# Optimization experiments

Measured on AMD Instinct MI355X. Metric: run time of the kernel, lower is better.

## Reference

```python
import jax, jax.numpy as jnp
import numpy as np

N_NODES = 50000
N_EDGES = 800000
D = 64  # in_dim = hidden = out_dim
LEAKY_SLOPE = 0.01  # F.leaky_relu default


def gat_layer(h, src, dst, W, b, aW, ab):
    # fc: z = h @ W.T + b            [N, D_out]
    z = h @ W.T + b
    zs = z[src]                       # gather src feats  [E, D_out]
    zd = z[dst]                       # gather dst feats  [E, D_out]
    # attn_fc(concat(z_src, z_dst)) -> scalar per edge, then leaky_relu
    e = jnp.concatenate([zs, zd], axis=-1) @ aW.T + ab   # [E, 1]
    e = jax.nn.leaky_relu(e, LEAKY_SLOPE)[:, 0]          # [E]
    # softmax over incoming edges per destination node (mailbox softmax)
    m = jax.ops.segment_max(e, dst, num_segments=N_NODES)    # [N]
    ex = jnp.exp(e - m[dst])
    den = jax.ops.segment_sum(ex, dst, num_segments=N_NODES)  # [N]
    alpha = ex / den[dst]                                      # [E]
    # scatter-sum aggregate of alpha * z_src
    return jax.ops.segment_sum(alpha[:, None] * zs, dst, num_segments=N_NODES)


def setup_inputs() -> dict:
    key = jax.random.key(0)
    ks = jax.random.split(key, 16)
    x = jax.random.normal(ks[0], (N_NODES, D), dtype=jnp.float32)
    src = jax.random.randint(ks[1], (N_EDGES,), 0, N_NODES)
    dst = jax.random.randint(ks[2], (N_EDGES,), 0, N_NODES)
    # xavier_normal with relu gain, per reset_parameters
    gain = float(np.sqrt(2.0))
    params = {}
    for i in range(3):
        std_fc = gain * np.sqrt(2.0 / (D + D))
        std_at = gain * np.sqrt(2.0 / (2 * D + 1))
        params[f"W{i}"] = jax.random.normal(ks[3 + 4 * i], (D, D), dtype=jnp.float32) * std_fc
        params[f"b{i}"] = jnp.zeros((D,), dtype=jnp.float32)
        params[f"a{i}"] = jax.random.normal(ks[4 + 4 * i], (1, 2 * D), dtype=jnp.float32) * std_at
        params[f"ab{i}"] = jnp.zeros((1,), dtype=jnp.float32)
    return {"x": x, "src": src, "dst": dst, **params}


def reference(x, src, dst, W0, b0, a0, ab0, W1, b1, a1, ab1, W2, b2, a2, ab2):
    h = gat_layer(x, src, dst, W0, b0, a0, ab0)
    h = jax.nn.relu(h)
    h = gat_layer(h, src, dst, W1, b1, a1, ab1)
    h = jax.nn.relu(h)
    h = gat_layer(h, src, dst, W2, b2, a2, ab2)
    return h
```

## Files before the change

kernel.cpp:

```cpp
#include <hip/hip_runtime.h>
#include <math.h>

#define N_NODES 50000
#define N_EDGES 800000
#define D 64

#define NB 256
#define NBLK 256
#define BUCKET_NODES 196
#define TILE 3125

template<int N>
__global__ void scan_partial_g(const int* __restrict__ in, int* __restrict__ partials) {
    const int base = blockIdx.x * 1024 + threadIdx.x * 4;
    int4 c = make_int4(0, 0, 0, 0);
    if (base + 3 < N) c = *(const int4*)&in[base];
    else { int* cp = (int*)&c; for (int j = 0; j < 4; ++j) if (base + j < N) cp[j] = in[base + j]; }
    int s = c.x + c.y + c.z + c.w;
    #pragma unroll
    for (int off = 32; off >= 1; off >>= 1) s += __shfl_xor(s, off, 64);
    __shared__ int red[4];
    if ((threadIdx.x & 63) == 0) red[threadIdx.x >> 6] = s;
    __syncthreads();
    if (threadIdx.x == 0) partials[blockIdx.x] = red[0] + red[1] + red[2] + red[3];
}

__global__ void scan_offsets_g(int* __restrict__ partials, int nt, int* __restrict__ total_out) {
    const int lane = threadIdx.x;
    const int v = (lane < nt) ? partials[lane] : 0;
    int inc = v;
    #pragma unroll
    for (int off = 1; off < 64; off <<= 1) {
        const int w = __shfl_up(inc, off, 64);
        if (lane >= off) inc += w;
    }
    if (lane < nt) partials[lane] = inc - v;
    if (total_out != nullptr && lane == 63) *total_out = inc;
}

template<int N>
__global__ void scan_write_g(const int* __restrict__ in, const int* __restrict__ partials,
                             int* __restrict__ out) {
    const int tid  = threadIdx.x;
    const int base = blockIdx.x * 1024 + tid * 4;
    int4 c = make_int4(0, 0, 0, 0);
    if (base + 3 < N) c = *(const int4*)&in[base];
    else { int* cp = (int*)&c; for (int j = 0; j < 4; ++j) if (base + j < N) cp[j] = in[base + j]; }
    const int s = c.x + c.y + c.z + c.w;
    __shared__ int sh[256];
    sh[tid] = s;
    __syncthreads();
    for (int off = 1; off < 256; off <<= 1) {
        const int w = (tid >= off) ? sh[tid - off] : 0;
        __syncthreads();
        sh[tid] += w;
        __syncthreads();
    }
    int run = partials[blockIdx.x] + sh[tid] - s;
    const int* cp = (const int*)&c;
    int rp[4];
    #pragma unroll
    for (int j = 0; j < 4; ++j) { rp[j] = run; run += cp[j]; }
    if (base + 3 < N) *(int4*)&out[base] = make_int4(rp[0], rp[1], rp[2], rp[3]);
    else for (int j = 0; j < 4; ++j) if (base + j < N) out[base + j] = rp[j];
}

__global__ __launch_bounds__(256) void bucket_hist(const int* __restrict__ dst,
                                                   int* __restrict__ Acnt) {
    __shared__ int hist[NB];
    for (int i = threadIdx.x; i < NB; i += 256) hist[i] = 0;
    __syncthreads();
    const int base = blockIdx.x * TILE;
    for (int i = threadIdx.x; i < TILE; i += 256)
        atomicAdd(&hist[dst[base + i] / BUCKET_NODES], 1);
    __syncthreads();
    for (int bk = threadIdx.x; bk < NB; bk += 256)
        Acnt[bk * NBLK + blockIdx.x] = hist[bk];
}

__global__ __launch_bounds__(256) void bucket_scatter(const int* __restrict__ src,
                                                      const int* __restrict__ dst,
                                                      const int* __restrict__ offs,
                                                      int2* __restrict__ staging) {
    __shared__ int cur[NB];
    for (int i = threadIdx.x; i < NB; i += 256) cur[i] = offs[i * NBLK + blockIdx.x];
    __syncthreads();
    const int base = blockIdx.x * TILE;
    for (int i = threadIdx.x; i < TILE; i += 256) {
        const int s = src[base + i], d = dst[base + i];
        const int pos = atomicAdd(&cur[d / BUCKET_NODES], 1);
        staging[pos] = make_int2(s, d);
    }
}

__global__ __launch_bounds__(256) void node_counts(const int2* __restrict__ staging,
                                                   const int* __restrict__ offs,
                                                   int* __restrict__ counts) {
    __shared__ int cnt[BUCKET_NODES];
    const int b = blockIdx.x;
    for (int i = threadIdx.x; i < BUCKET_NODES; i += 256) cnt[i] = 0;
    __syncthreads();
    const int s0 = offs[b * NBLK];
    const int s1 = (b == NB - 1) ? N_EDGES : offs[(b + 1) * NBLK];
    for (int i = s0 + threadIdx.x; i < s1; i += 256)
        atomicAdd(&cnt[staging[i].y - b * BUCKET_NODES], 1);
    __syncthreads();
    for (int i = threadIdx.x; i < BUCKET_NODES; i += 256) {
        const int node = b * BUCKET_NODES + i;
        if (node < N_NODES) counts[node] = cnt[i];
    }
}

__global__ __launch_bounds__(256) void bucket_to_csr(const int2* __restrict__ staging,
                                                     const int* __restrict__ offs,
                                                     const int* __restrict__ row_ptr,
                                                     int* __restrict__ csr_src) {
    __shared__ int cur[BUCKET_NODES];
    const int b = blockIdx.x;
    for (int i = threadIdx.x; i < BUCKET_NODES; i += 256) {
        const int node = b * BUCKET_NODES + i;
        cur[i] = (node < N_NODES) ? row_ptr[node] : 0;
    }
    __syncthreads();
    const int s0 = offs[b * NBLK];
    const int s1 = (b == NB - 1) ? N_EDGES : offs[(b + 1) * NBLK];
    for (int i = s0 + threadIdx.x; i < s1; i += 256) {
        const int2 e = staging[i];
        const int pos = atomicAdd(&cur[e.y - b * BUCKET_NODES], 1);
        csr_src[pos] = e.x;
    }
}

__global__ void hist_kernel(const int* __restrict__ dst, int* __restrict__ counts) {
    const int i = blockIdx.x * blockDim.x + threadIdx.x;
    if (i < N_EDGES) atomicAdd(&counts[dst[i]], 1);
}
__global__ void copy_kernel(const int* __restrict__ in, int* __restrict__ out, int n) {
    const int i = blockIdx.x * blockDim.x + threadIdx.x;
    if (i < n) out[i] = in[i];
}
__global__ void scatter_kernel(const int* __restrict__ src, const int* __restrict__ dst,
                               int* __restrict__ cursor, int* __restrict__ csr_src) {
    const int i = blockIdx.x * blockDim.x + threadIdx.x;
    if (i >= N_EDGES) return;
    const int pos = atomicAdd(&cursor[dst[i]], 1);
    csr_src[pos] = src[i];
}

#define NL_ROWS 8
__global__ __launch_bounds__(256) void node_linear_gemm(
    const float* __restrict__ h, float* __restrict__ z,
    const float* __restrict__ W, const float* __restrict__ b,
    const float* __restrict__ a, const float* __restrict__ ab,
    float* __restrict__ s_src, float* __restrict__ s_dst)
{
    __shared__ float Wt[64 * 65];
    for (int idx = threadIdx.x; idx < D * D; idx += 256) {
        const int j = idx >> 6, k = idx & 63;
        Wt[k * 65 + j] = W[idx];
    }
    __syncthreads();

    const int lane = threadIdx.x & 63;
    const int wv   = __builtin_amdgcn_readfirstlane(threadIdx.x >> 6);
    const int row0 = (blockIdx.x * 4 + wv) * NL_ROWS;
    if (row0 >= N_NODES) return;

    const float bj  = b[lane];
    const float alo = a[lane];
    const float ahi = a[64 + lane];

    const float* hr[NL_ROWS];
    #pragma unroll
    for (int r = 0; r < NL_ROWS; ++r) hr[r] = h + (size_t)(row0 + r) * D;

    float acc[NL_ROWS];
    #pragma unroll
    for (int r = 0; r < NL_ROWS; ++r) acc[r] = bj;

    #pragma unroll 4
    for (int k = 0; k < D; ++k) {
        const float wkj = Wt[k * 65 + lane];
        #pragma unroll
        for (int r = 0; r < NL_ROWS; ++r)
            acc[r] = fmaf(hr[r][k], wkj, acc[r]);
    }

    #pragma unroll
    for (int r = 0; r < NL_ROWS; ++r) {
        z[(size_t)(row0 + r) * D + lane] = acc[r];
        float u = acc[r] * alo;
        float v = acc[r] * ahi;
        #pragma unroll
        for (int off = 32; off >= 1; off >>= 1) {
            u += __shfl_xor(u, off, 64);
            v += __shfl_xor(v, off, 64);
        }
        if (lane == 0) { s_src[row0 + r] = u; s_dst[row0 + r] = v + ab[0]; }
    }
}

template<bool RELU>
__global__ __launch_bounds__(256) void gat_aggregate(
    const int* __restrict__ row_ptr, const int* __restrict__ csr_src,
    const float* __restrict__ s_src, const float* __restrict__ s_dst,
    const float* __restrict__ z, float* __restrict__ out)
{
    __shared__ float sh_ex[4][64];
    __shared__ int   sh_si[4][64];
    const int lane = threadIdx.x & 63;
    const int wv   = threadIdx.x >> 6;
    const int node = blockIdx.x * 4 + wv;
    if (node >= N_NODES) return;
    const int beg = row_ptr[node];
    const int end = row_ptr[node + 1];
    if (beg == end) { out[(size_t)node * D + lane] = 0.f; return; }
    const float sd = s_dst[node];

    float m = -INFINITY;
    float den = 0.f;
    float a0 = 0.f, a1 = 0.f, a2 = 0.f, a3 = 0.f;
    float a4 = 0.f, a5 = 0.f, a6 = 0.f, a7 = 0.f;

    for (int base = beg; base < end; base += 64) {
        const int n = min(64, end - base);
        const int sidx = (lane < n) ? csr_src[base + lane] : 0;
        float e = -INFINITY;
        if (lane < n) {
            e = s_src[sidx] + sd;
            e = e > 0.f ? e : 0.01f * e;
        }
        float mc = e;
        #pragma unroll
        for (int off = 32; off >= 1; off >>= 1) mc = fmaxf(mc, __shfl_xor(mc, off, 64));
        if (mc > m) {
            const float scale = __expf(m - mc);
            den *= scale;
            a0 *= scale; a1 *= scale; a2 *= scale; a3 *= scale;
            a4 *= scale; a5 *= scale; a6 *= scale; a7 *= scale;
            m = mc;
        }
        const float ex = __expf(e - m);
        den += ex;
        sh_ex[wv][lane] = ex;
        sh_si[wv][lane] = sidx;
        const int nn = (n + 7) & ~7;
        for (int t = 0; t < nn; t += 8) {
            const float4 w0 = *(const float4*)&sh_ex[wv][t];
            const float4 w1 = *(const float4*)&sh_ex[wv][t + 4];
            const int4   s0 = *(const int4*)  &sh_si[wv][t];
            const int4   s1 = *(const int4*)  &sh_si[wv][t + 4];
            const float z0 = z[(size_t)s0.x * D + lane];
            const float z1 = z[(size_t)s0.y * D + lane];
            const float z2 = z[(size_t)s0.z * D + lane];
            const float z3 = z[(size_t)s0.w * D + lane];
            const float z4 = z[(size_t)s1.x * D + lane];
            const float z5 = z[(size_t)s1.y * D + lane];
            const float z6 = z[(size_t)s1.z * D + lane];
            const float z7 = z[(size_t)s1.w * D + lane];
            a0 = fmaf(w0.x, z0, a0);
            a1 = fmaf(w0.y, z1, a1);
            a2 = fmaf(w0.z, z2, a2);
            a3 = fmaf(w0.w, z3, a3);
            a4 = fmaf(w1.x, z4, a4);
            a5 = fmaf(w1.y, z5, a5);
            a6 = fmaf(w1.z, z6, a6);
            a7 = fmaf(w1.w, z7, a7);
        }
    }
    #pragma unroll
    for (int off = 32; off >= 1; off >>= 1) den += __shfl_xor(den, off, 64);
    float v = (((a0 + a1) + (a2 + a3)) + ((a4 + a5) + (a6 + a7))) / den;
    if (RELU) v = fmaxf(v, 0.f);
    out[(size_t)node * D + lane] = v;
}

extern "C" void kernel_launch(void* const* d_in, const int* in_sizes, int n_in,
                              void* d_out, int out_size, void* d_ws, size_t ws_size,
                              hipStream_t stream) {
    const float* x   = (const float*)d_in[0];
    const int*   src = (const int*)d_in[1];
    const int*   dst = (const int*)d_in[2];
    float* out = (float*)d_out;

    char* wp = (char*)d_ws;
    auto alloc = [&](size_t bytes) -> void* {
        void* p = (void*)wp;
        wp += (bytes + 255) & ~(size_t)255;
        return p;
    };
    float* zbuf    = (float*)alloc((size_t)N_NODES * D * sizeof(float));
    float* s_src   = (float*)alloc((size_t)N_NODES * sizeof(float));
    float* s_dst   = (float*)alloc((size_t)N_NODES * sizeof(float));
    int*   counts  = (int*)alloc((size_t)N_NODES * sizeof(int));
    int*   row_ptr = (int*)alloc((size_t)(N_NODES + 1) * sizeof(int));
    int*   csr_src = (int*)alloc((size_t)N_EDGES * sizeof(int));
    int*   partA   = (int*)alloc(64 * sizeof(int));
    int*   partB   = (int*)alloc(64 * sizeof(int));
    int*   cursor  = (int*)alloc((size_t)N_NODES * sizeof(int));
    size_t base_used = (size_t)(wp - (char*)d_ws);
    int*   Acnt    = (int*)alloc((size_t)NB * NBLK * sizeof(int));
    int*   offs    = (int*)alloc((size_t)NB * NBLK * sizeof(int));
    int2*  staging = (int2*)alloc((size_t)N_EDGES * sizeof(int2));
    size_t bucket_used = (size_t)(wp - (char*)d_ws);

    const bool use_bucket = (ws_size >= bucket_used);
    (void)base_used;

    if (use_bucket) {
        bucket_hist<<<NBLK, 256, 0, stream>>>(dst, Acnt);
        scan_partial_g<NB * NBLK><<<64, 256, 0, stream>>>(Acnt, partB);
        scan_offsets_g<<<1, 64, 0, stream>>>(partB, 64, nullptr);
        scan_write_g<NB * NBLK><<<64, 256, 0, stream>>>(Acnt, partB, offs);
        bucket_scatter<<<NBLK, 256, 0, stream>>>(src, dst, offs, staging);
        node_counts<<<NB, 256, 0, stream>>>(staging, offs, counts);
        scan_partial_g<N_NODES><<<49, 256, 0, stream>>>(counts, partA);
        scan_offsets_g<<<1, 64, 0, stream>>>(partA, 49, &row_ptr[N_NODES]);
        scan_write_g<N_NODES><<<49, 256, 0, stream>>>(counts, partA, row_ptr);
        bucket_to_csr<<<NB, 256, 0, stream>>>(staging, offs, row_ptr, csr_src);
    } else {
        hipMemsetAsync(counts, 0, (size_t)N_NODES * sizeof(int), stream);
        hist_kernel<<<(N_EDGES + 255) / 256, 256, 0, stream>>>(dst, counts);
        scan_partial_g<N_NODES><<<49, 256, 0, stream>>>(counts, partA);
        scan_offsets_g<<<1, 64, 0, stream>>>(partA, 49, &row_ptr[N_NODES]);
        scan_write_g<N_NODES><<<49, 256, 0, stream>>>(counts, partA, row_ptr);
        copy_kernel<<<(N_NODES + 255) / 256, 256, 0, stream>>>(row_ptr, cursor, N_NODES);
        scatter_kernel<<<(N_EDGES + 255) / 256, 256, 0, stream>>>(src, dst, cursor, csr_src);
    }

    const int grid_k1  = (N_NODES + 4 * NL_ROWS - 1) / (4 * NL_ROWS);
    const int grid_agg = (N_NODES + 3) / 4;

    for (int layer = 0; layer < 3; ++layer) {
        const float* W  = (const float*)d_in[3 + 4 * layer];
        const float* b  = (const float*)d_in[4 + 4 * layer];
        const float* a  = (const float*)d_in[5 + 4 * layer];
        const float* ab = (const float*)d_in[6 + 4 * layer];
        const float* hin = (layer == 0) ? x : out;

        node_linear_gemm<<<grid_k1, 256, 0, stream>>>(hin, zbuf, W, b, a, ab, s_src, s_dst);
        if (layer < 2) {
            gat_aggregate<true ><<<grid_agg, 256, 0, stream>>>(row_ptr, csr_src, s_src, s_dst, zbuf, out);
        } else {
            gat_aggregate<false><<<grid_agg, 256, 0, stream>>>(row_ptr, csr_src, s_src, s_dst, zbuf, out);
        }
    }
}
```

Before: 215.5 us.

## Store node features as bf16 and gather two edges per wavefront pass

The linear kernel now writes z as bf16 with round-to-nearest-even instead of fp32. The aggregation kernel has each half-wavefront read a 4-byte pair of bf16 features per lane, so one wavefront handles two edges per gather instruction, and the halves are combined with a cross-half shuffle at the end. This halves the bytes moved in the random-access gather of z, which dominates aggregation. The cost is reduced precision in the aggregated features (attention scores stay fp32), and the output error may grow across the three layers.

```diff
diff --git a/kernel.cpp b/kernel.cpp
--- a/kernel.cpp
+++ b/kernel.cpp
@@ -9,6 +9,14 @@
 #define NBLK 256
 #define BUCKET_NODES 196
 #define TILE 3125
+
+typedef unsigned short ushort_t;
+
+__device__ __forceinline__ ushort_t f32_to_bf16(float f) {
+    unsigned u = __float_as_uint(f);
+    u += 0x7fffu + ((u >> 16) & 1u);
+    return (ushort_t)(u >> 16);
+}
 
 template<int N>
 __global__ void scan_partial_g(const int* __restrict__ in, int* __restrict__ partials) {
@@ -149,7 +157,7 @@
 
 #define NL_ROWS 8
 __global__ __launch_bounds__(256) void node_linear_gemm(
-    const float* __restrict__ h, float* __restrict__ z,
+    const float* __restrict__ h, ushort_t* __restrict__ zb,
     const float* __restrict__ W, const float* __restrict__ b,
     const float* __restrict__ a, const float* __restrict__ ab,
     float* __restrict__ s_src, float* __restrict__ s_dst)
@@ -188,7 +196,7 @@
 
     #pragma unroll
     for (int r = 0; r < NL_ROWS; ++r) {
-        z[(size_t)(row0 + r) * D + lane] = acc[r];
+        zb[(size_t)(row0 + r) * D + lane] = f32_to_bf16(acc[r]);
         float u = acc[r] * alo;
         float v = acc[r] * ahi;
         #pragma unroll
@@ -204,7 +212,7 @@
 __global__ __launch_bounds__(256) void gat_aggregate(
     const int* __restrict__ row_ptr, const int* __restrict__ csr_src,
     const float* __restrict__ s_src, const float* __restrict__ s_dst,
-    const float* __restrict__ z, float* __restrict__ out)
+    const ushort_t* __restrict__ zb, float* __restrict__ out)
 {
     __shared__ float sh_ex[4][64];
     __shared__ int   sh_si[4][64];
@@ -215,12 +223,15 @@
     const int beg = row_ptr[node];
     const int end = row_ptr[node + 1];
     if (beg == end) { out[(size_t)node * D + lane] = 0.f; return; }
+    const int half = lane >> 5;
+    const int fl   = lane & 31;
     const float sd = s_dst[node];
 
     float m = -INFINITY;
     float den = 0.f;
-    float a0 = 0.f, a1 = 0.f, a2 = 0.f, a3 = 0.f;
-    float a4 = 0.f, a5 = 0.f, a6 = 0.f, a7 = 0.f;
+    float2 acc[8];
+    #pragma unroll
+    for (int p = 0; p < 8; ++p) acc[p] = make_float2(0.f, 0.f);
 
     for (int base = beg; base < end; base += 64) {
         const int n = min(64, end - base);
@@ -236,43 +247,39 @@
         if (mc > m) {
             const float scale = __expf(m - mc);
             den *= scale;
-            a0 *= scale; a1 *= scale; a2 *= scale; a3 *= scale;
-            a4 *= scale; a5 *= scale; a6 *= scale; a7 *= scale;
+            #pragma unroll
+            for (int p = 0; p < 8; ++p) { acc[p].x *= scale; acc[p].y *= scale; }
             m = mc;
         }
         const float ex = __expf(e - m);
         den += ex;
         sh_ex[wv][lane] = ex;
         sh_si[wv][lane] = sidx;
-        const int nn = (n + 7) & ~7;
-        for (int t = 0; t < nn; t += 8) {
-            const float4 w0 = *(const float4*)&sh_ex[wv][t];
-            const float4 w1 = *(const float4*)&sh_ex[wv][t + 4];
-            const int4   s0 = *(const int4*)  &sh_si[wv][t];
-            const int4   s1 = *(const int4*)  &sh_si[wv][t + 4];
-            const float z0 = z[(size_t)s0.x * D + lane];
-            const float z1 = z[(size_t)s0.y * D + lane];
-            const float z2 = z[(size_t)s0.z * D + lane];
-            const float z3 = z[(size_t)s0.w * D + lane];
-            const float z4 = z[(size_t)s1.x * D + lane];
-            const float z5 = z[(size_t)s1.y * D + lane];
-            const float z6 = z[(size_t)s1.z * D + lane];
-            const float z7 = z[(size_t)s1.w * D + lane];
-            a0 = fmaf(w0.x, z0, a0);
-            a1 = fmaf(w0.y, z1, a1);
-            a2 = fmaf(w0.z, z2, a2);
-            a3 = fmaf(w0.w, z3, a3);
-            a4 = fmaf(w1.x, z4, a4);
-            a5 = fmaf(w1.y, z5, a5);
-            a6 = fmaf(w1.z, z6, a6);
-            a7 = fmaf(w1.w, z7, a7);
+        for (int t = 0; t < n; t += 16) {
+            #pragma unroll
+            for (int p = 0; p < 8; ++p) {
+                const int ei = t + 2 * p + half;
+                const float w = sh_ex[wv][ei];
+                const int   s = sh_si[wv][ei];
+                const unsigned u = *(const unsigned*)&zb[(size_t)s * D + 2 * fl];
+                const float f0 = __uint_as_float(u << 16);
+                const float f1 = __uint_as_float(u & 0xffff0000u);
+                acc[p].x = fmaf(w, f0, acc[p].x);
+                acc[p].y = fmaf(w, f1, acc[p].y);
+            }
         }
     }
     #pragma unroll
     for (int off = 32; off >= 1; off >>= 1) den += __shfl_xor(den, off, 64);
-    float v = (((a0 + a1) + (a2 + a3)) + ((a4 + a5) + (a6 + a7))) / den;
-    if (RELU) v = fmaxf(v, 0.f);
-    out[(size_t)node * D + lane] = v;
+    float2 tot = make_float2(0.f, 0.f);
+    #pragma unroll
+    for (int p = 0; p < 8; ++p) { tot.x += acc[p].x; tot.y += acc[p].y; }
+    tot.x += __shfl_xor(tot.x, 32, 64);
+    tot.y += __shfl_xor(tot.y, 32, 64);
+    float2 v = make_float2(tot.x / den, tot.y / den);
+    if (RELU) { v.x = fmaxf(v.x, 0.f); v.y = fmaxf(v.y, 0.f); }
+    if (half == 0)
+        *(float2*)&out[(size_t)node * D + 2 * fl] = v;
 }
 
 extern "C" void kernel_launch(void* const* d_in, const int* in_sizes, int n_in,
@@ -289,7 +296,7 @@
         wp += (bytes + 255) & ~(size_t)255;
         return p;
     };
-    float* zbuf    = (float*)alloc((size_t)N_NODES * D * sizeof(float));
+    ushort_t* zb    = (ushort_t*)alloc((size_t)N_NODES * D * sizeof(ushort_t));
     float* s_src   = (float*)alloc((size_t)N_NODES * sizeof(float));
     float* s_dst   = (float*)alloc((size_t)N_NODES * sizeof(float));
     int*   counts  = (int*)alloc((size_t)N_NODES * sizeof(int));
@@ -298,14 +305,12 @@
     int*   partA   = (int*)alloc(64 * sizeof(int));
     int*   partB   = (int*)alloc(64 * sizeof(int));
     int*   cursor  = (int*)alloc((size_t)N_NODES * sizeof(int));
-    size_t base_used = (size_t)(wp - (char*)d_ws);
     int*   Acnt    = (int*)alloc((size_t)NB * NBLK * sizeof(int));
     int*   offs    = (int*)alloc((size_t)NB * NBLK * sizeof(int));
     int2*  staging = (int2*)alloc((size_t)N_EDGES * sizeof(int2));
     size_t bucket_used = (size_t)(wp - (char*)d_ws);
 
     const bool use_bucket = (ws_size >= bucket_used);
-    (void)base_used;
 
     if (use_bucket) {
         bucket_hist<<<NBLK, 256, 0, stream>>>(dst, Acnt);
@@ -338,11 +343,11 @@
         const float* ab = (const float*)d_in[6 + 4 * layer];
         const float* hin = (layer == 0) ? x : out;
 
-        node_linear_gemm<<<grid_k1, 256, 0, stream>>>(hin, zbuf, W, b, a, ab, s_src, s_dst);
+        node_linear_gemm<<<grid_k1, 256, 0, stream>>>(hin, zb, W, b, a, ab, s_src, s_dst);
         if (layer < 2) {
-            gat_aggregate<true ><<<grid_agg, 256, 0, stream>>>(row_ptr, csr_src, s_src, s_dst, zbuf, out);
+            gat_aggregate<true ><<<grid_agg, 256, 0, stream>>>(row_ptr, csr_src, s_src, s_dst, zb, out);
         } else {
-            gat_aggregate<false><<<grid_agg, 256, 0, stream>>>(row_ptr, csr_src, s_src, s_dst, zbuf, out);
-        }
-    }
-}
+            gat_aggregate<false><<<grid_agg, 256, 0, stream>>>(row_ptr, csr_src, s_src, s_dst, zb, out);
+        }
+    }
+}
```

Result: slower. 220.2 us (+2.2%).
